# Kernel tuning notes

Measured on AMD Instinct MI355X. Metric: run time of the kernel, lower is better.

The kernel has to match this reference:

```python
import jax, jax.numpy as jnp
import numpy as np

E = 1024  # embedding_size
H = 16    # multi_head_num


def setup_inputs() -> dict:
    key = jax.random.key(0)
    ks = jax.random.split(key, 9)
    B, N = 4, 1024
    s = 1.0 / np.sqrt(E)
    return {
        "x": jax.random.normal(ks[0], (B, N, E), dtype=jnp.float32),
        "Wq": jax.random.normal(ks[1], (E, E), dtype=jnp.float32) * s,
        "bq": jax.random.normal(ks[2], (E,), dtype=jnp.float32) * 0.02,
        "Wk": jax.random.normal(ks[3], (E, E), dtype=jnp.float32) * s,
        "bk": jax.random.normal(ks[4], (E,), dtype=jnp.float32) * 0.02,
        "Wv": jax.random.normal(ks[5], (E, E), dtype=jnp.float32) * s,
        "bv": jax.random.normal(ks[6], (E,), dtype=jnp.float32) * 0.02,
        "Wo": jax.random.normal(ks[7], (E, E), dtype=jnp.float32) * s,
        "bo": jax.random.normal(ks[8], (E,), dtype=jnp.float32) * 0.02,
    }


def reference(x, Wq, bq, Wk, bk, Wv, bv, Wo, bo):
    B, N, _ = x.shape
    d = E // H

    def heads(y):  # [B,N,E] -> [B,H,N,d]
        return y.reshape(B, N, H, d).transpose(0, 2, 1, 3)

    q = heads(x @ Wq.T + bq)
    k = heads(x @ Wk.T + bk)
    v = heads(x @ Wv.T + bv)

    energy = jnp.einsum('bhqd,bhkd->bhqk', q, k)
    # NOTE: module divides by sqrt(E) AFTER softmax (faithful to source)
    scaling = jnp.asarray(E, x.dtype) ** 0.5
    att = jax.nn.softmax(energy, axis=-1) / scaling
    out = jnp.einsum('bhal,bhlv->bhav', att, v)
    out = out.transpose(0, 2, 1, 3).reshape(B, N, E)
    return out @ Wo.T + bo
```

## Files before the change

### kernel.cpp

```cpp
#include <hip/hip_runtime.h>
#include <hip/hip_bf16.h>


typedef __bf16 bf16x8 __attribute__((ext_vector_type(8)));
typedef __bf16 bf16x4 __attribute__((ext_vector_type(4)));
typedef float  f32x4  __attribute__((ext_vector_type(4)));

#define LOG2E 1.44269504f

__device__ __forceinline__ void glds16(const __bf16* g, __bf16* l) {
  __builtin_amdgcn_global_load_lds(
      (const __attribute__((address_space(1))) void*)g,
      (__attribute__((address_space(3))) void*)l, 16, 0, 0);
}

__global__ __launch_bounds__(256) void cvt_f32_bf16(const float* __restrict__ in,
                                                    __bf16* __restrict__ out, int n4) {
  int i = blockIdx.x * 256 + threadIdx.x;
  if (i < n4) {
    float4 v = *(const float4*)(in + (size_t)i * 4);
    bf16x4 b = {(__bf16)v.x, (__bf16)v.y, (__bf16)v.z, (__bf16)v.w};
    *(bf16x4*)(out + (size_t)i * 4) = b;
  }
}

__global__ __launch_bounds__(256) void cvt_all(const float* __restrict__ x,
                                               const float* __restrict__ Wq,
                                               const float* __restrict__ Wk,
                                               const float* __restrict__ Wv,
                                               const float* __restrict__ Wo,
                                               __bf16* __restrict__ xb,
                                               __bf16* __restrict__ Wqb,
                                               __bf16* __restrict__ Wkb,
                                               __bf16* __restrict__ Wvb,
                                               __bf16* __restrict__ Wob) {
  const int i = blockIdx.x * 256 + threadIdx.x;
  const float* src;
  __bf16* dst;
  int off;
  if (i < 1048576) {
    src = x; dst = xb; off = i;
  } else {
    const int j = i - 1048576;
    const int seg = j >> 18;
    off = j & 262143;
    src = (seg == 0) ? Wq : (seg == 1) ? Wk : (seg == 2) ? Wv : Wo;
    dst = (seg == 0) ? Wqb : (seg == 1) ? Wkb : (seg == 2) ? Wvb : Wob;
  }
  float4 v = *(const float4*)(src + (size_t)off * 4);
  bf16x4 b = {(__bf16)v.x, (__bf16)v.y, (__bf16)v.z, (__bf16)v.w};
  *(bf16x4*)(dst + (size_t)off * 4) = b;
}

template <bool WBF16>
__global__ __launch_bounds__(256, 3) void gemm_qkv(const __bf16* __restrict__ A,
                                                   const void* __restrict__ Wqp,
                                                   const void* __restrict__ Wkp,
                                                   const void* __restrict__ Wvp,
                                                   const float* __restrict__ bq,
                                                   const float* __restrict__ bk,
                                                   const float* __restrict__ bv,
                                                   __bf16* __restrict__ Qw,
                                                   __bf16* __restrict__ Kw,
                                                   __bf16* __restrict__ Vw) {
  constexpr int BST = WBF16 ? 64 : 72;
  __shared__ __attribute__((aligned(16))) __bf16 As[128][64];
  __shared__ __attribute__((aligned(16))) __bf16 Bs[128 * BST];

  const int tid = threadIdx.x;
  const int lane = tid & 63, w = tid >> 6;
  const int wm = w >> 1, wn = w & 1;
  const int l15 = lane & 15, lq = lane >> 4;
  const int lr = lane >> 3, lc = lane & 7;
  const int xs = l15 & 7;

  const int bid = blockIdx.x;
  const int c = bid & 7, t = bid >> 3;
  const int z = t >> 5;
  const int r = t & 31;
  const int nb = r & 7;
  const int mb = c * 4 + (r >> 3);
  const int m0 = mb * 128, n0 = nb * 128;

  const void* Wp = (z == 0) ? Wqp : (z == 1) ? Wkp : Wvp;
  const float* bias = (z == 0) ? bq : (z == 1) ? bk : bv;
  __bf16* C = (z == 0) ? Qw : (z == 1) ? Kw : Vw;
  const float scale = (z == 0) ? LOG2E : 1.0f;

  f32x4 acc[4][4] = {};

  for (int k0 = 0; k0 < 1024; k0 += 64) {
#pragma unroll
    for (int i = 0; i < 4; ++i) {
      const int row = w * 32 + i * 8 + lr;
      glds16(A + (size_t)(m0 + row) * 1024 + k0 + ((lc ^ lr) * 8), &As[row][lc * 8]);
    }
    if (WBF16) {
      const __bf16* Wb = (const __bf16*)Wp;
#pragma unroll
      for (int i = 0; i < 4; ++i) {
        const int row = w * 32 + i * 8 + lr;
        glds16(Wb + (size_t)(n0 + row) * 1024 + k0 + ((lc ^ lr) * 8), &Bs[row * 64 + lc * 8]);
      }
    } else {
      const float* W = (const float*)Wp;
#pragma unroll
      for (int i = 0; i < 8; ++i) {
        const int cc = i * 256 + tid, row = cc >> 4, col = (cc & 15) * 4;
        float4 wv = *(const float4*)(W + (size_t)(n0 + row) * 1024 + k0 + col);
        bf16x4 b4 = {(__bf16)wv.x, (__bf16)wv.y, (__bf16)wv.z, (__bf16)wv.w};
        *(bf16x4*)(&Bs[row * 72 + col]) = b4;
      }
    }
    __syncthreads();
#pragma unroll
    for (int s = 0; s < 2; ++s) {
      bf16x8 af[4], bfv[4];
#pragma unroll
      for (int mt = 0; mt < 4; ++mt)
        af[mt] = *(const bf16x8*)(&As[wm * 64 + mt * 16 + l15][((s * 4 + lq) ^ xs) * 8]);
#pragma unroll
      for (int nt = 0; nt < 4; ++nt) {
        const int row = wn * 64 + nt * 16 + l15;
        if (WBF16)
          bfv[nt] = *(const bf16x8*)(&Bs[row * 64 + (((s * 4 + lq) ^ xs) * 8)]);
        else
          bfv[nt] = *(const bf16x8*)(&Bs[row * 72 + s * 32 + lq * 8]);
      }
#pragma unroll
      for (int mt = 0; mt < 4; ++mt)
#pragma unroll
        for (int nt = 0; nt < 4; ++nt)
          acc[mt][nt] = __builtin_amdgcn_mfma_f32_16x16x32_bf16(
              af[mt], bfv[nt], acc[mt][nt], 0, 0, 0);
    }
    __syncthreads();
  }

#pragma unroll
  for (int mt = 0; mt < 4; ++mt) {
    const int mg_base = m0 + wm * 64 + mt * 16 + lq * 4;
    const int bb = mg_base >> 10, nr0 = mg_base & 1023;
#pragma unroll
    for (int nt = 0; nt < 4; ++nt) {
      const int ng = n0 + wn * 64 + nt * 16 + l15;
      const float bv = bias[ng];
      const int h = ng >> 6, dd = ng & 63;
      if (z != 2) {
#pragma unroll
        for (int rr = 0; rr < 4; ++rr) {
          const int mg = mg_base + rr;
          const size_t idx =
              ((size_t)(bb * 16 + h) << 16) + (size_t)(mg & 1023) * 64 + dd;
          C[idx] = (__bf16)((acc[mt][nt][rr] + bv) * scale);
        }
      } else {
        bf16x4 o4 = {(__bf16)(acc[mt][nt][0] + bv), (__bf16)(acc[mt][nt][1] + bv),
                     (__bf16)(acc[mt][nt][2] + bv), (__bf16)(acc[mt][nt][3] + bv)};
        *(bf16x4*)(&C[((size_t)(bb * 16 + h) << 16) + (size_t)dd * 1024 + nr0]) = o4;
      }
    }
  }
}

__global__ __launch_bounds__(256) void gemm_out(const __bf16* __restrict__ A,
                                                const __bf16* __restrict__ W,
                                                const float* __restrict__ bias,
                                                float* __restrict__ C) {
  __shared__ __attribute__((aligned(16))) __bf16 As[64][64];
  __shared__ __attribute__((aligned(16))) __bf16 Bs[128][64];

  const int tid = threadIdx.x;
  const int lane = tid & 63, w = tid >> 6;
  const int wm = w >> 1, wn = w & 1;
  const int l15 = lane & 15, lq = lane >> 4;
  const int lr = lane >> 3, lc = lane & 7;
  const int xs = l15 & 7;

  const int bid = blockIdx.x;
  const int c = bid & 7, t = bid >> 3;
  const int mb = c * 8 + (t & 7);
  const int nb = t >> 3;
  const int m0 = mb * 64, n0 = nb * 128;

  f32x4 acc[2][4] = {};

  for (int k0 = 0; k0 < 1024; k0 += 64) {
#pragma unroll
    for (int i = 0; i < 2; ++i) {
      const int row = w * 16 + i * 8 + lr;
      glds16(A + (size_t)(m0 + row) * 1024 + k0 + ((lc ^ lr) * 8), &As[row][lc * 8]);
    }
#pragma unroll
    for (int i = 0; i < 4; ++i) {
      const int row = w * 32 + i * 8 + lr;
      glds16(W + (size_t)(n0 + row) * 1024 + k0 + ((lc ^ lr) * 8), &Bs[row][lc * 8]);
    }
    __syncthreads();
#pragma unroll
    for (int s = 0; s < 2; ++s) {
      bf16x8 af[2], bfv[4];
#pragma unroll
      for (int mt = 0; mt < 2; ++mt)
        af[mt] = *(const bf16x8*)(&As[wm * 32 + mt * 16 + l15][((s * 4 + lq) ^ xs) * 8]);
#pragma unroll
      for (int nt = 0; nt < 4; ++nt)
        bfv[nt] = *(const bf16x8*)(&Bs[wn * 64 + nt * 16 + l15][((s * 4 + lq) ^ xs) * 8]);
#pragma unroll
      for (int mt = 0; mt < 2; ++mt)
#pragma unroll
        for (int nt = 0; nt < 4; ++nt)
          acc[mt][nt] = __builtin_amdgcn_mfma_f32_16x16x32_bf16(
              af[mt], bfv[nt], acc[mt][nt], 0, 0, 0);
    }
    __syncthreads();
  }

#pragma unroll
  for (int mt = 0; mt < 2; ++mt) {
    const int mg_base = m0 + wm * 32 + mt * 16 + lq * 4;
#pragma unroll
    for (int nt = 0; nt < 4; ++nt) {
      const int ng = n0 + wn * 64 + nt * 16 + l15;
      const float bv = bias[ng];
#pragma unroll
      for (int r = 0; r < 4; ++r)
        C[(size_t)(mg_base + r) * 1024 + ng] = acc[mt][nt][r] + bv;
    }
  }
}

__global__ __launch_bounds__(256) void attn_kernel(const __bf16* __restrict__ Q,
                                                   const __bf16* __restrict__ K,
                                                   const __bf16* __restrict__ Vt,
                                                   __bf16* __restrict__ O) {
  __shared__ __attribute__((aligned(16))) __bf16 PQ[9216];
  __shared__ __attribute__((aligned(16))) __bf16 Ks[64][64];
  __shared__ __attribute__((aligned(16))) __bf16 Vs[64][64];

  __bf16(*Qst)[64] = (__bf16(*)[64])PQ;
  __bf16(*Ps)[32][72] = (__bf16(*)[32][72])PQ;

  const int tid = threadIdx.x;
  const int lane = tid & 63, w = tid >> 6;
  const int l15 = lane & 15, lq = lane >> 4;
  const int lr = lane >> 3, lc = lane & 7;
  const int xs = l15 & 7;

  const int bh = blockIdx.x;
  const int qt = blockIdx.y;
  const __bf16* Qh = Q + (size_t)bh * 65536;
  const __bf16* Kh = K + (size_t)bh * 65536;
  const __bf16* Vh = Vt + (size_t)bh * 65536;

#pragma unroll
  for (int i = 0; i < 4; ++i) {
    const int row = w * 32 + i * 8 + lr;
    glds16(Qh + (size_t)(qt * 128 + row) * 64 + ((lc ^ lr) * 8), &Qst[row][lc * 8]);
  }
  __syncthreads();
  bf16x8 bqr[2][2];
#pragma unroll
  for (int nq = 0; nq < 2; ++nq)
#pragma unroll
    for (int s = 0; s < 2; ++s)
      bqr[nq][s] = *(const bf16x8*)(&Qst[w * 32 + nq * 16 + l15][((s * 4 + lq) ^ xs) * 8]);

  float l_run[2] = {0.0f, 0.0f};
  f32x4 oacc[2][4] = {};

  for (int kb = 0; kb < 16; ++kb) {
#pragma unroll
    for (int i = 0; i < 2; ++i) {
      const int row = w * 16 + i * 8 + lr;
      glds16(Kh + (size_t)kb * 4096 + (size_t)row * 64 + ((lc ^ lr) * 8), &Ks[row][lc * 8]);
      glds16(Vh + (size_t)row * 1024 + kb * 64 + ((lc ^ lr) * 8), &Vs[row][lc * 8]);
    }
    __syncthreads();

    f32x4 sacc[2][4] = {};
#pragma unroll
    for (int s = 0; s < 2; ++s) {
#pragma unroll
      for (int mt = 0; mt < 4; ++mt) {
        bf16x8 ak = *(const bf16x8*)(&Ks[mt * 16 + l15][((s * 4 + lq) ^ xs) * 8]);
#pragma unroll
        for (int nq = 0; nq < 2; ++nq)
          sacc[nq][mt] = __builtin_amdgcn_mfma_f32_16x16x32_bf16(
              ak, bqr[nq][s], sacc[nq][mt], 0, 0, 0);
      }
    }

#pragma unroll
    for (int nq = 0; nq < 2; ++nq) {
      float sum = 0.0f;
#pragma unroll
      for (int mt = 0; mt < 4; ++mt)
#pragma unroll
        for (int r = 0; r < 4; ++r) {
          const float e = __builtin_amdgcn_exp2f(sacc[nq][mt][r]);
          sacc[nq][mt][r] = e;
          sum += e;
        }
      sum += __shfl_xor(sum, 16, 64);
      sum += __shfl_xor(sum, 32, 64);
      l_run[nq] += sum;
    }

#pragma unroll
    for (int nq = 0; nq < 2; ++nq)
#pragma unroll
      for (int mt = 0; mt < 4; ++mt) {
        bf16x4 p4 = {(__bf16)sacc[nq][mt][0], (__bf16)sacc[nq][mt][1],
                     (__bf16)sacc[nq][mt][2], (__bf16)sacc[nq][mt][3]};
        *(bf16x4*)(&Ps[w][nq * 16 + l15][mt * 16 + lq * 4]) = p4;
      }
    __threadfence_block();

#pragma unroll
    for (int s = 0; s < 2; ++s) {
      bf16x8 bp[2];
#pragma unroll
      for (int nq = 0; nq < 2; ++nq)
        bp[nq] = *(const bf16x8*)(&Ps[w][nq * 16 + l15][s * 32 + lq * 8]);
#pragma unroll
      for (int mt = 0; mt < 4; ++mt) {
        bf16x8 av = *(const bf16x8*)(&Vs[mt * 16 + l15][((s * 4 + lq) ^ xs) * 8]);
#pragma unroll
        for (int nq = 0; nq < 2; ++nq)
          oacc[nq][mt] = __builtin_amdgcn_mfma_f32_16x16x32_bf16(
              av, bp[nq], oacc[nq][mt], 0, 0, 0);
      }
    }
    __syncthreads();
  }

  const int b = bh >> 4, h = bh & 15;
#pragma unroll
  for (int nq = 0; nq < 2; ++nq) {
    const float inv = 1.0f / (l_run[nq] * 32.0f);
    const size_t base =
        (size_t)(b * 1024 + qt * 128 + w * 32 + nq * 16 + l15) * 1024 + h * 64;
#pragma unroll
    for (int mt = 0; mt < 4; ++mt) {
      bf16x4 o4 = {(__bf16)(oacc[nq][mt][0] * inv), (__bf16)(oacc[nq][mt][1] * inv),
                   (__bf16)(oacc[nq][mt][2] * inv), (__bf16)(oacc[nq][mt][3] * inv)};
      *(bf16x4*)(&O[base + mt * 16 + lq * 4]) = o4;
    }
  }
}

extern "C" void kernel_launch(void* const* d_in, const int* in_sizes, int n_in,
                              void* d_out, int out_size, void* d_ws, size_t ws_size,
                              hipStream_t stream) {
  const float* x  = (const float*)d_in[0];
  const float* Wq = (const float*)d_in[1];
  const float* bq = (const float*)d_in[2];
  const float* Wk = (const float*)d_in[3];
  const float* bk = (const float*)d_in[4];
  const float* Wv = (const float*)d_in[5];
  const float* bv = (const float*)d_in[6];
  const float* Wo = (const float*)d_in[7];
  const float* bo = (const float*)d_in[8];
  float* out = (float*)d_out;

  const size_t SZ = (size_t)4 * 1024 * 1024;
  __bf16* Qw = (__bf16*)d_ws;
  __bf16* Kw = Qw + SZ;
  __bf16* Vw = Kw + SZ;
  __bf16* s3 = Vw + SZ;
  __bf16* xb = s3;
  __bf16* Ow = s3;

  dim3 blk(256);

  if (ws_size >= (size_t)40 * 1024 * 1024) {
    __bf16* Wqb = s3 + SZ;
    __bf16* Wkb = Wqb + SZ / 4;
    __bf16* Wvb = Wkb + SZ / 4;
    __bf16* Wob = Wvb + SZ / 4;
    cvt_all<<<8192, blk, 0, stream>>>(x, Wq, Wk, Wv, Wo, xb, Wqb, Wkb, Wvb, Wob);
    gemm_qkv<true><<<dim3(768), blk, 0, stream>>>(xb, Wqb, Wkb, Wvb,
                                                  bq, bk, bv, Qw, Kw, Vw);
    attn_kernel<<<dim3(64, 8), blk, 0, stream>>>(Qw, Kw, Vw, Ow);
    gemm_out<<<dim3(512), blk, 0, stream>>>(Ow, Wob, bo, out);
  } else {
    __bf16* Wob = Kw;
    cvt_f32_bf16<<<4096, blk, 0, stream>>>(x, xb, 1048576);
    gemm_qkv<false><<<dim3(768), blk, 0, stream>>>(xb, Wq, Wk, Wv,
                                                   bq, bk, bv, Qw, Kw, Vw);
    attn_kernel<<<dim3(64, 8), blk, 0, stream>>>(Qw, Kw, Vw, Ow);
    cvt_f32_bf16<<<1024, blk, 0, stream>>>(Wo, Wob, 262144);
    gemm_out<<<dim3(512), blk, 0, stream>>>(Ow, Wob, bo, out);
  }
}
```

Baseline: 164.6 us.

## Triple-buffer LDS in attention and output GEMM with async prefetch

Both the attention kernel and the output projection GEMM move to dynamic shared memory with three LDS slots and prefetch tiles two iterations ahead using global_load_lds. Explicit vmcnt waits and a single barrier per iteration replace the two __syncthreads per iteration, and MFMA sections are wrapped in setprio raises. The aim is to hide global load latency behind compute, at the cost of much larger LDS per block (~66-72 KB), which may lower occupancy. The dynamic shared memory limits are set once through a static flag.

```diff
diff --git a/kernel.cpp b/kernel.cpp
--- a/kernel.cpp
+++ b/kernel.cpp
@@ -163,12 +163,13 @@
   }
 }
 
-__global__ __launch_bounds__(256) void gemm_out(const __bf16* __restrict__ A,
-                                                const __bf16* __restrict__ W,
-                                                const float* __restrict__ bias,
-                                                float* __restrict__ C) {
-  __shared__ __attribute__((aligned(16))) __bf16 As[64][64];
-  __shared__ __attribute__((aligned(16))) __bf16 Bs[128][64];
+__global__ __launch_bounds__(256, 2) void gemm_out(const __bf16* __restrict__ A,
+                                                   const __bf16* __restrict__ W,
+                                                   const float* __restrict__ bias,
+                                                   float* __restrict__ C) {
+  extern __shared__ __attribute__((aligned(16))) __bf16 lds_o[];
+  __bf16(*As)[64][64] = (__bf16(*)[64][64])lds_o;
+  __bf16(*Bs)[128][64] = (__bf16(*)[128][64])(lds_o + 12288);
 
   const int tid = threadIdx.x;
   const int lane = tid & 63, w = tid >> 6;
@@ -183,37 +184,52 @@
   const int nb = t >> 3;
   const int m0 = mb * 64, n0 = nb * 128;
 
-  f32x4 acc[2][4] = {};
-
-  for (int k0 = 0; k0 < 1024; k0 += 64) {
+  auto stage = [&](int kb, int sl) {
+    const int k0 = kb * 64;
 #pragma unroll
     for (int i = 0; i < 2; ++i) {
       const int row = w * 16 + i * 8 + lr;
-      glds16(A + (size_t)(m0 + row) * 1024 + k0 + ((lc ^ lr) * 8), &As[row][lc * 8]);
+      glds16(A + (size_t)(m0 + row) * 1024 + k0 + ((lc ^ lr) * 8), &As[sl][row][lc * 8]);
     }
 #pragma unroll
     for (int i = 0; i < 4; ++i) {
       const int row = w * 32 + i * 8 + lr;
-      glds16(W + (size_t)(n0 + row) * 1024 + k0 + ((lc ^ lr) * 8), &Bs[row][lc * 8]);
-    }
-    __syncthreads();
+      glds16(W + (size_t)(n0 + row) * 1024 + k0 + ((lc ^ lr) * 8), &Bs[sl][row][lc * 8]);
+    }
+  };
+
+  f32x4 acc[2][4] = {};
+
+  stage(0, 0);
+  stage(1, 1);
+
+  for (int kb = 0; kb < 16; ++kb) {
+    if (kb < 15)
+      asm volatile("s_waitcnt vmcnt(6)" ::: "memory");
+    else
+      asm volatile("s_waitcnt vmcnt(0)" ::: "memory");
+    __builtin_amdgcn_s_barrier();
+    if (kb < 14) stage(kb + 2, (kb + 2) % 3);
+
+    const int sl = kb % 3;
 #pragma unroll
     for (int s = 0; s < 2; ++s) {
       bf16x8 af[2], bfv[4];
 #pragma unroll
       for (int mt = 0; mt < 2; ++mt)
-        af[mt] = *(const bf16x8*)(&As[wm * 32 + mt * 16 + l15][((s * 4 + lq) ^ xs) * 8]);
+        af[mt] = *(const bf16x8*)(&As[sl][wm * 32 + mt * 16 + l15][((s * 4 + lq) ^ xs) * 8]);
 #pragma unroll
       for (int nt = 0; nt < 4; ++nt)
-        bfv[nt] = *(const bf16x8*)(&Bs[wn * 64 + nt * 16 + l15][((s * 4 + lq) ^ xs) * 8]);
+        bfv[nt] = *(const bf16x8*)(&Bs[sl][wn * 64 + nt * 16 + l15][((s * 4 + lq) ^ xs) * 8]);
+      __builtin_amdgcn_s_setprio(1);
 #pragma unroll
       for (int mt = 0; mt < 2; ++mt)
 #pragma unroll
         for (int nt = 0; nt < 4; ++nt)
           acc[mt][nt] = __builtin_amdgcn_mfma_f32_16x16x32_bf16(
               af[mt], bfv[nt], acc[mt][nt], 0, 0, 0);
-    }
-    __syncthreads();
+      __builtin_amdgcn_s_setprio(0);
+    }
   }
 
 #pragma unroll
@@ -230,14 +246,14 @@
   }
 }
 
-__global__ __launch_bounds__(256) void attn_kernel(const __bf16* __restrict__ Q,
-                                                   const __bf16* __restrict__ K,
-                                                   const __bf16* __restrict__ Vt,
-                                                   __bf16* __restrict__ O) {
-  __shared__ __attribute__((aligned(16))) __bf16 PQ[9216];
-  __shared__ __attribute__((aligned(16))) __bf16 Ks[64][64];
-  __shared__ __attribute__((aligned(16))) __bf16 Vs[64][64];
-
+__global__ __launch_bounds__(256, 2) void attn_kernel(const __bf16* __restrict__ Q,
+                                                      const __bf16* __restrict__ K,
+                                                      const __bf16* __restrict__ Vt,
+                                                      __bf16* __restrict__ O) {
+  extern __shared__ __attribute__((aligned(16))) __bf16 lds_a[];
+  __bf16(*Ks)[64][64] = (__bf16(*)[64][64])lds_a;
+  __bf16(*Vs)[64][64] = (__bf16(*)[64][64])(lds_a + 12288);
+  __bf16* PQ = lds_a + 24576;
   __bf16(*Qst)[64] = (__bf16(*)[64])PQ;
   __bf16(*Ps)[32][72] = (__bf16(*)[32][72])PQ;
 
@@ -253,11 +269,23 @@
   const __bf16* Kh = K + (size_t)bh * 65536;
   const __bf16* Vh = Vt + (size_t)bh * 65536;
 
+  auto stage_kv = [&](int kb, int sl) {
+#pragma unroll
+    for (int i = 0; i < 2; ++i) {
+      const int row = w * 16 + i * 8 + lr;
+      glds16(Kh + (size_t)kb * 4096 + (size_t)row * 64 + ((lc ^ lr) * 8),
+             &Ks[sl][row][lc * 8]);
+      glds16(Vh + (size_t)row * 1024 + kb * 64 + ((lc ^ lr) * 8),
+             &Vs[sl][row][lc * 8]);
+    }
+  };
+
 #pragma unroll
   for (int i = 0; i < 4; ++i) {
     const int row = w * 32 + i * 8 + lr;
     glds16(Qh + (size_t)(qt * 128 + row) * 64 + ((lc ^ lr) * 8), &Qst[row][lc * 8]);
   }
+  stage_kv(0, 0);
   __syncthreads();
   bf16x8 bqr[2][2];
 #pragma unroll
@@ -265,31 +293,35 @@
 #pragma unroll
     for (int s = 0; s < 2; ++s)
       bqr[nq][s] = *(const bf16x8*)(&Qst[w * 32 + nq * 16 + l15][((s * 4 + lq) ^ xs) * 8]);
+  __syncthreads();
+  stage_kv(1, 1);
 
   float l_run[2] = {0.0f, 0.0f};
   f32x4 oacc[2][4] = {};
 
   for (int kb = 0; kb < 16; ++kb) {
-#pragma unroll
-    for (int i = 0; i < 2; ++i) {
-      const int row = w * 16 + i * 8 + lr;
-      glds16(Kh + (size_t)kb * 4096 + (size_t)row * 64 + ((lc ^ lr) * 8), &Ks[row][lc * 8]);
-      glds16(Vh + (size_t)row * 1024 + kb * 64 + ((lc ^ lr) * 8), &Vs[row][lc * 8]);
-    }
-    __syncthreads();
+    if (kb < 15)
+      asm volatile("s_waitcnt vmcnt(4)" ::: "memory");
+    else
+      asm volatile("s_waitcnt vmcnt(0)" ::: "memory");
+    __builtin_amdgcn_s_barrier();
+    if (kb < 14) stage_kv(kb + 2, (kb + 2) % 3);
+    const int sl = kb % 3;
 
     f32x4 sacc[2][4] = {};
+    __builtin_amdgcn_s_setprio(1);
 #pragma unroll
     for (int s = 0; s < 2; ++s) {
 #pragma unroll
       for (int mt = 0; mt < 4; ++mt) {
-        bf16x8 ak = *(const bf16x8*)(&Ks[mt * 16 + l15][((s * 4 + lq) ^ xs) * 8]);
+        bf16x8 ak = *(const bf16x8*)(&Ks[sl][mt * 16 + l15][((s * 4 + lq) ^ xs) * 8]);
 #pragma unroll
         for (int nq = 0; nq < 2; ++nq)
           sacc[nq][mt] = __builtin_amdgcn_mfma_f32_16x16x32_bf16(
               ak, bqr[nq][s], sacc[nq][mt], 0, 0, 0);
       }
     }
+    __builtin_amdgcn_s_setprio(0);
 
 #pragma unroll
     for (int nq = 0; nq < 2; ++nq) {
@@ -317,6 +349,7 @@
       }
     __threadfence_block();
 
+    __builtin_amdgcn_s_setprio(1);
 #pragma unroll
     for (int s = 0; s < 2; ++s) {
       bf16x8 bp[2];
@@ -325,14 +358,14 @@
         bp[nq] = *(const bf16x8*)(&Ps[w][nq * 16 + l15][s * 32 + lq * 8]);
 #pragma unroll
       for (int mt = 0; mt < 4; ++mt) {
-        bf16x8 av = *(const bf16x8*)(&Vs[mt * 16 + l15][((s * 4 + lq) ^ xs) * 8]);
+        bf16x8 av = *(const bf16x8*)(&Vs[sl][mt * 16 + l15][((s * 4 + lq) ^ xs) * 8]);
 #pragma unroll
         for (int nq = 0; nq < 2; ++nq)
           oacc[nq][mt] = __builtin_amdgcn_mfma_f32_16x16x32_bf16(
               av, bp[nq], oacc[nq][mt], 0, 0, 0);
       }
     }
-    __syncthreads();
+    __builtin_amdgcn_s_setprio(0);
   }
 
   const int b = bh >> 4, h = bh & 15;
@@ -374,6 +407,15 @@
 
   dim3 blk(256);
 
+  static bool attr_set = false;
+  if (!attr_set) {
+    (void)hipFuncSetAttribute((const void*)attn_kernel,
+                              hipFuncAttributeMaxDynamicSharedMemorySize, 67584);
+    (void)hipFuncSetAttribute((const void*)gemm_out,
+                              hipFuncAttributeMaxDynamicSharedMemorySize, 73728);
+    attr_set = true;
+  }
+
   if (ws_size >= (size_t)40 * 1024 * 1024) {
     __bf16* Wqb = s3 + SZ;
     __bf16* Wkb = Wqb + SZ / 4;
@@ -382,15 +424,15 @@
     cvt_all<<<8192, blk, 0, stream>>>(x, Wq, Wk, Wv, Wo, xb, Wqb, Wkb, Wvb, Wob);
     gemm_qkv<true><<<dim3(768), blk, 0, stream>>>(xb, Wqb, Wkb, Wvb,
                                                   bq, bk, bv, Qw, Kw, Vw);
-    attn_kernel<<<dim3(64, 8), blk, 0, stream>>>(Qw, Kw, Vw, Ow);
-    gemm_out<<<dim3(512), blk, 0, stream>>>(Ow, Wob, bo, out);
+    attn_kernel<<<dim3(64, 8), blk, 67584, stream>>>(Qw, Kw, Vw, Ow);
+    gemm_out<<<dim3(512), blk, 73728, stream>>>(Ow, Wob, bo, out);
   } else {
     __bf16* Wob = Kw;
     cvt_f32_bf16<<<4096, blk, 0, stream>>>(x, xb, 1048576);
     gemm_qkv<false><<<dim3(768), blk, 0, stream>>>(xb, Wq, Wk, Wv,
                                                    bq, bk, bv, Qw, Kw, Vw);
-    attn_kernel<<<dim3(64, 8), blk, 0, stream>>>(Qw, Kw, Vw, Ow);
+    attn_kernel<<<dim3(64, 8), blk, 67584, stream>>>(Qw, Kw, Vw, Ow);
     cvt_f32_bf16<<<1024, blk, 0, stream>>>(Wo, Wob, 262144);
-    gemm_out<<<dim3(512), blk, 0, stream>>>(Ow, Wob, bo, out);
-  }
-}
+    gemm_out<<<dim3(512), blk, 73728, stream>>>(Ow, Wob, bo, out);
+  }
+}
```

Measured after the change: 161.1 us, median of 2. 2.1% less time.
